# Kernel optimization log

Hardware: AMD Instinct MI355X
Metric: run time of the kernel (lower is better)

Reference implementation:

```python
import jax, jax.numpy as jnp
import numpy as np

B, N_LR, N_HR = 2, 8192, 16384
C = 32          # feature channels (query_ch = neigh_ch = 32 in Grouper7)
NSAMPLE = 64    # nsamples=[64]
RADIUS = 1.0    # radius=[1.0]
LR_VOX = np.array([0.4, 0.4, 1.0], np.float32)   # lr_voxel_size (x,y,z)
HR_VOX = np.array([0.05, 0.05, 0.1], np.float32) # hr_voxel_size (x,y,z)
OFFSET = np.array([0.0, -40.0, -3.0], np.float32)


def setup_inputs() -> dict:
    key = jax.random.key(0)
    ks = jax.random.split(key, 6)
    lr_idx = jax.random.randint(ks[0], (B, N_LR, 3), 0, 25, dtype=jnp.int32)    # (z,y,x) voxel coords
    hr_idx = jax.random.randint(ks[1], (B, N_HR, 3), 0, 200, dtype=jnp.int32)
    lr_feat = jax.random.normal(ks[2], (B, N_LR, C), jnp.float32)
    hr_feat = jax.random.normal(ks[3], (B, N_HR, C), jnp.float32)
    # Grouper7 MLP [[32,32]] on use_xyz-augmented neighbor feats (3+C -> 32 -> 32), bn=False
    W1 = jax.random.normal(ks[4], (C + 3, C), jnp.float32) * 0.1
    b1 = jnp.zeros((C,), jnp.float32)
    W2 = jax.random.normal(ks[5], (C, C), jnp.float32) * 0.1
    b2 = jnp.zeros((C,), jnp.float32)
    return dict(lr_idx=lr_idx, hr_idx=hr_idx, lr_feat=lr_feat, hr_feat=hr_feat,
                W1=W1, b1=b1, W2=W2, b2=b2)


def _to_xyz(idx, vox, off):
    # spconv indices are (z,y,x); code does indices[:, [3,2,1]] * voxel_size + offset + 0.5*voxel_size
    return idx[..., ::-1].astype(jnp.float32) * vox + off + 0.5 * vox


def _group_one(lr_xyz, hr_xyz, hr_f, W1, b1, W2, b2):
    # ball query: first NSAMPLE hr points within RADIUS of each lr query point
    d2 = jnp.sum((lr_xyz[:, None, :] - hr_xyz[None, :, :]) ** 2, axis=-1)  # [N_lr, N_hr]
    mask = d2 <= RADIUS ** 2
    order = jnp.where(mask, -jnp.arange(hr_xyz.shape[0], dtype=jnp.float32), -jnp.inf)
    _, idx = jax.lax.top_k(order, NSAMPLE)            # lowest valid indices first (PointNet++ semantics)
    valid = jnp.take_along_axis(mask, idx, axis=1)
    first = jnp.where(valid[:, :1], idx[:, :1], 0)
    idx = jnp.where(valid, idx, first)                # pad empty slots with first valid neighbor (0 if none)
    rel = hr_xyz[idx] - lr_xyz[:, None, :]            # [N_lr, ns, 3] relative coords (use_xyz=True)
    g = jnp.concatenate([rel, hr_f[idx]], axis=-1)    # [N_lr, ns, 3+C]
    h = jax.nn.relu(g @ W1 + b1)                      # shared 1x1-conv MLP, bn=False
    h = jax.nn.relu(h @ W2 + b2)
    return h.max(axis=1)                              # max-pool over neighbors -> [N_lr, C]


def reference(lr_idx, hr_idx, lr_feat, hr_feat, W1, b1, W2, b2):
    vox_lr = jnp.asarray(LR_VOX)
    vox_hr = jnp.asarray(HR_VOX)
    off = jnp.asarray(OFFSET)
    lr_xyz = _to_xyz(lr_idx, vox_lr, off)             # [B, N_lr, 3]
    hr_xyz = _to_xyz(hr_idx, vox_hr, off)             # [B, N_hr, 3]
    new = jax.vmap(_group_one, in_axes=(0, 0, 0, None, None, None, None))(
        lr_xyz, hr_xyz, hr_feat, W1, b1, W2, b2)      # [B, N_lr, C]
    # structured_forward: torch.cat([lr_features, new_lr_features], dim=-1)
    return jnp.concatenate([lr_feat, new], axis=-1)   # [B, N_lr, 2C]
```

## Files before the change

### kernel.cpp

```cpp
#include <hip/hip_runtime.h>
#include <cstdint>
#include <cstddef>
#include <climits>

constexpr int B_   = 2;
constexpr int NLR  = 8192;
constexpr int NHR  = 16384;
constexpr int CCH  = 32;
constexpr int NS   = 64;
constexpr int THREADS = 256;

constexpr int GX = 11, GY = 11, GZ = 20;
constexpr int NCELLS = GX * GY * GZ;
constexpr int NCT    = B_ * NCELLS;
constexpr int CAP    = 192;
constexpr float SCALE = 0.999f;

__device__ __forceinline__ float cvt_coord(int i, float vox, float off) {
    return __fadd_rn(__fadd_rn(__fmul_rn((float)i, vox), off), __fmul_rn(0.5f, vox));
}

__device__ __forceinline__ void hr_coords(const int* ip, float& x, float& y, float& z) {
    x = cvt_coord(ip[2], 0.05f,   0.0f);
    y = cvt_coord(ip[1], 0.05f, -40.0f);
    z = cvt_coord(ip[0], 0.1f,   -3.0f);
}

__device__ __forceinline__ int cell_of(float x, float y, float z) {
    const int cx = (int)(__fmul_rn(x, SCALE));
    const int cy = (int)(__fmul_rn(__fadd_rn(y, 40.0f), SCALE));
    const int cz = (int)(__fmul_rn(__fadd_rn(z,  3.0f), SCALE));
    return (cz * GY + cy) * GX + cx;
}

extern "C" __global__ void k_hist(const int* __restrict__ hr_idx, int* __restrict__ cnt) {
    const int gid = blockIdx.x * THREADS + threadIdx.x;
    const int b = gid >> 14;
    const int* ip = hr_idx + (size_t)gid * 3;
    float x, y, z;
    hr_coords(ip, x, y, z);
    atomicAdd(&cnt[b * NCELLS + cell_of(x, y, z)], 1);
}

extern "C" __global__ void k_scan(const int* __restrict__ cnt, int* __restrict__ start,
                                  int* __restrict__ cursor) {
    __shared__ int sums[THREADS];
    constexpr int CH = (NCT + THREADS - 1) / THREADS;
    const int t = threadIdx.x;
    int loc[CH];
    int s = 0;
#pragma unroll
    for (int k = 0; k < CH; ++k) {
        const int i = t * CH + k;
        loc[k] = s;
        s += (i < NCT) ? cnt[i] : 0;
    }
    sums[t] = s;
    __syncthreads();
    for (int off = 1; off < THREADS; off <<= 1) {
        const int v = (t >= off) ? sums[t - off] : 0;
        __syncthreads();
        sums[t] += v;
        __syncthreads();
    }
    const int pre = (t > 0) ? sums[t - 1] : 0;
#pragma unroll
    for (int k = 0; k < CH; ++k) {
        const int i = t * CH + k;
        if (i < NCT) {
            const int st = pre + loc[k];
            start[i]  = st;
            cursor[i] = st;
        }
    }
    if (t == THREADS - 1) start[NCT] = sums[THREADS - 1];
}

extern "C" __global__ void k_scatter(const int* __restrict__ hr_idx, int* __restrict__ cursor,
                                     float4* __restrict__ pts) {
    const int gid = blockIdx.x * THREADS + threadIdx.x;
    const int b = gid >> 14;
    const int i = gid & (NHR - 1);
    const int* ip = hr_idx + (size_t)gid * 3;
    float x, y, z;
    hr_coords(ip, x, y, z);
    const int c = b * NCELLS + cell_of(x, y, z);
    const int slot = atomicAdd(&cursor[c], 1);
    float4 v;
    v.x = x; v.y = y; v.z = z; v.w = __int_as_float(i);
    pts[slot] = v;
}

extern "C" __global__ void __launch_bounds__(THREADS)
__attribute__((amdgpu_waves_per_eu(2, 4)))
k_group(const int* __restrict__ lr_idx, const int* __restrict__ hr_idx,
        const float* __restrict__ lr_feat, const float* __restrict__ hr_feat,
        const float* __restrict__ W1, const float* __restrict__ b1,
        const float* __restrict__ W2, const float* __restrict__ b2,
        const int* __restrict__ start, const float4* __restrict__ pts,
        float* __restrict__ out)
{
    __shared__ int cand[4][CAP];

    const int tid  = threadIdx.x;
    const int wave = tid >> 6;
    const int lane = tid & 63;
    const int q    = blockIdx.x * 4 + wave;
    const int b    = q >> 13;

    const int* qip = lr_idx + (size_t)q * 3;
    const float qx = cvt_coord(qip[2], 0.4f,   0.0f);
    const float qy = cvt_coord(qip[1], 0.4f, -40.0f);
    const float qz = cvt_coord(qip[0], 1.0f,  -3.0f);

    const int cqx = (int)(__fmul_rn(qx, SCALE));
    const int cqy = (int)(__fmul_rn(__fadd_rn(qy, 40.0f), SCALE));
    const int cqz = (int)(__fmul_rn(__fadd_rn(qz,  3.0f), SCALE));
    const int x0 = max(cqx - 1, 0), x1 = min(cqx + 1, GX - 1);
    const int y0 = max(cqy - 1, 0), y1 = min(cqy + 1, GY - 1);
    const int z0 = max(cqz - 1, 0), z1 = min(cqz + 1, GZ - 1);
    const int nx = x1 - x0 + 1;
    const int bbase = b * NCELLS;

    int cnt = 0;
    for (int zz = z0; zz <= z1; ++zz)
    for (int yy = y0; yy <= y1; ++yy) {
        const int g0 = bbase + (zz * GY + yy) * GX + x0;
        const int s  = start[g0];
        const int e  = start[g0 + nx];
        for (int base = s; base < e; base += 64) {
            const int j = base + lane;
            bool ok = false;
            int id = 0;
            if (j < e) {
                const float4 pv = pts[j];
                const float dx = __fsub_rn(qx, pv.x);
                const float dy = __fsub_rn(qy, pv.y);
                const float dz = __fsub_rn(qz, pv.z);
                const float d2 = __fadd_rn(__fadd_rn(__fmul_rn(dx, dx),
                                                     __fmul_rn(dy, dy)),
                                           __fmul_rn(dz, dz));
                ok = d2 <= 1.0f;
                id = __float_as_int(pv.w);
            }
            const unsigned long long m = __ballot(ok);
            if (m != 0ull) {
                const int before = (int)__popcll(m & ((1ull << lane) - 1ull));
                const int pos = cnt + before;
                if (ok && pos < CAP) cand[wave][pos] = id;
                cnt += (int)__popcll(m);
                if (cnt > CAP) cnt = CAP;
            }
        }
    }

    int pid;
    if (cnt <= NS) {
        int myid = (lane < cnt) ? cand[wave][lane] : INT_MAX;
        int mp = myid;
#pragma unroll
        for (int s = 32; s >= 1; s >>= 1) mp = min(mp, __shfl_xor(mp, s, 64));
        pid = (lane < cnt) ? myid : ((cnt > 0) ? mp : 0);
    } else {
        const int c = cnt;
        int mine = 0;
        for (int k = 0; k < NS; ++k) {
            int lm = INT_MAX;
            for (int j = lane; j < c; j += 64) lm = min(lm, cand[wave][j]);
#pragma unroll
            for (int s = 32; s >= 1; s >>= 1) lm = min(lm, __shfl_xor(lm, s, 64));
            for (int j = lane; j < c; j += 64)
                if (cand[wave][j] == lm) cand[wave][j] = INT_MAX;
            if (lane == k) mine = lm;
        }
        pid = mine;
    }

    const int* ip = hr_idx + ((size_t)b * NHR + pid) * 3;
    float px, py, pz;
    hr_coords(ip, px, py, pz);

    float g[3 + CCH];
    g[0] = __fsub_rn(px, qx);
    g[1] = __fsub_rn(py, qy);
    g[2] = __fsub_rn(pz, qz);
    const float4* fp = reinterpret_cast<const float4*>(hr_feat + ((size_t)b * NHR + pid) * CCH);
#pragma unroll
    for (int k = 0; k < CCH / 4; ++k) {
        const float4 v = fp[k];
        g[3 + 4 * k + 0] = v.x;
        g[3 + 4 * k + 1] = v.y;
        g[3 + 4 * k + 2] = v.z;
        g[3 + 4 * k + 3] = v.w;
    }

    float h[32];
#pragma unroll 32
    for (int j = 0; j < 32; ++j) h[j] = b1[j];
#pragma unroll 35
    for (int k = 0; k < 35; ++k) {
        const float gk = g[k];
#pragma unroll 32
        for (int j = 0; j < 32; ++j)
            h[j] = fmaf(gk, W1[k * 32 + j], h[j]);
    }
#pragma unroll 32
    for (int j = 0; j < 32; ++j) h[j] = fmaxf(h[j], 0.0f);

    float h2[32];
#pragma unroll 32
    for (int j = 0; j < 32; ++j) h2[j] = b2[j];
#pragma unroll 32
    for (int k = 0; k < 32; ++k) {
        const float hk = h[k];
#pragma unroll 32
        for (int j = 0; j < 32; ++j)
            h2[j] = fmaf(hk, W2[k * 32 + j], h2[j]);
    }
#pragma unroll 32
    for (int j = 0; j < 32; ++j) h2[j] = fmaxf(h2[j], 0.0f);

#pragma unroll
    for (int s = 32; s >= 1; s >>= 1) {
#pragma unroll 32
        for (int j = 0; j < 32; ++j)
            h2[j] = fmaxf(h2[j], __shfl_xor(h2[j], s, 64));
    }

    float* orow = out + (size_t)q * (2 * CCH);
    if (lane < CCH)
        orow[lane] = lr_feat[(size_t)q * CCH + lane];
    if (lane == 0) {
#pragma unroll
        for (int j = 0; j < 8; ++j) {
            float4 v;
            v.x = h2[4 * j + 0];
            v.y = h2[4 * j + 1];
            v.z = h2[4 * j + 2];
            v.w = h2[4 * j + 3];
            reinterpret_cast<float4*>(orow + CCH)[j] = v;
        }
    }
}

extern "C" void kernel_launch(void* const* d_in, const int* in_sizes, int n_in,
                              void* d_out, int out_size, void* d_ws, size_t ws_size,
                              hipStream_t stream) {
    const int*   lr_idx  = (const int*)  d_in[0];
    const int*   hr_idx  = (const int*)  d_in[1];
    const float* lr_feat = (const float*)d_in[2];
    const float* hr_feat = (const float*)d_in[3];
    const float* W1      = (const float*)d_in[4];
    const float* b1      = (const float*)d_in[5];
    const float* W2      = (const float*)d_in[6];
    const float* b2      = (const float*)d_in[7];
    float* out = (float*)d_out;

    int*    cell_count  = (int*)d_ws;
    int*    cell_start  = cell_count + NCT;
    int*    cell_cursor = cell_start + (NCT + 1);
    size_t  off = ((size_t)(3 * NCT + 1) * sizeof(int) + 15) & ~(size_t)15;
    float4* pts = (float4*)((char*)d_ws + off);

    hipMemsetAsync(cell_count, 0, NCT * sizeof(int), stream);

    const dim3 blk(THREADS);
    hipLaunchKernelGGL(k_hist,    dim3(B_ * NHR / THREADS), blk, 0, stream, hr_idx, cell_count);
    hipLaunchKernelGGL(k_scan,    dim3(1),                  blk, 0, stream, cell_count, cell_start, cell_cursor);
    hipLaunchKernelGGL(k_scatter, dim3(B_ * NHR / THREADS), blk, 0, stream, hr_idx, cell_cursor, pts);
    hipLaunchKernelGGL(k_group,   dim3(B_ * NLR / 4),       blk, 0, stream,
                       lr_idx, hr_idx, lr_feat, hr_feat, W1, b1, W2, b2,
                       cell_start, pts, out);
}
```

Before: 177.3 us.

## Run grouper MLP on bf16 MFMA with LDS-staged swizzled operands

Replaces the per-lane scalar FP32 two-layer MLP (35x32 and 32x32 FMAs per neighbor plus a 32-channel shuffle max-reduction) with bf16 16x16x32 MFMA tiles. Weights are converted to bf16 and laid out in LDS in fragment order, and gathered neighbor features and hidden activations are staged in XOR-swizzled LDS buffers. The max-pool then reduces only two values per lane across 4 row groups. This removes most VALU work and register pressure, at the cost of bf16 precision on inputs and activations and more LDS use. The waves-per-eu hint is also dropped.

```diff
diff --git a/kernel.cpp b/kernel.cpp
--- a/kernel.cpp
+++ b/kernel.cpp
@@ -1,4 +1,5 @@
 #include <hip/hip_runtime.h>
+#include <hip/hip_bf16.h>
 #include <cstdint>
 #include <cstddef>
 #include <climits>
@@ -16,6 +17,9 @@
 constexpr int CAP    = 192;
 constexpr float SCALE = 0.999f;
 
+typedef __attribute__((ext_vector_type(8))) short bf16x8;
+typedef __attribute__((ext_vector_type(4))) float f32x4;
+
 __device__ __forceinline__ float cvt_coord(int i, float vox, float off) {
     return __fadd_rn(__fadd_rn(__fmul_rn((float)i, vox), off), __fmul_rn(0.5f, vox));
 }
@@ -31,6 +35,11 @@
     const int cy = (int)(__fmul_rn(__fadd_rn(y, 40.0f), SCALE));
     const int cz = (int)(__fmul_rn(__fadd_rn(z,  3.0f), SCALE));
     return (cz * GY + cy) * GX + cx;
+}
+
+__device__ __forceinline__ unsigned short f2bf(float f) {
+    __hip_bfloat16 h = __float2bfloat16(f);
+    return __builtin_bit_cast(unsigned short, h);
 }
 
 extern "C" __global__ void k_hist(const int* __restrict__ hr_idx, int* __restrict__ cnt) {
@@ -92,7 +101,6 @@
 }
 
 extern "C" __global__ void __launch_bounds__(THREADS)
-__attribute__((amdgpu_waves_per_eu(2, 4)))
 k_group(const int* __restrict__ lr_idx, const int* __restrict__ hr_idx,
         const float* __restrict__ lr_feat, const float* __restrict__ hr_feat,
         const float* __restrict__ W1, const float* __restrict__ b1,
@@ -100,6 +108,11 @@
         const int* __restrict__ start, const float4* __restrict__ pts,
         float* __restrict__ out)
 {
+    __shared__ __align__(16) unsigned short W1f[2][2][64][8];
+    __shared__ __align__(16) unsigned short W2f[2][64][8];
+    __shared__ __align__(16) unsigned short Xf[4][64][32];
+    __shared__ __align__(16) unsigned short XYZ[4][64][4];
+    __shared__ __align__(16) unsigned short Hb[4][64][32];
     __shared__ int cand[4][CAP];
 
     const int tid  = threadIdx.x;
@@ -107,6 +120,32 @@
     const int lane = tid & 63;
     const int q    = blockIdx.x * 4 + wave;
     const int b    = q >> 13;
+
+#pragma unroll
+    for (int e = 0; e < 8; ++e) {
+        const int flat = tid * 8 + e;
+        const int j  = flat & 7;
+        const int l  = (flat >> 3) & 63;
+        const int ct = (flat >> 9) & 1;
+        const int ks = (flat >> 10) & 1;
+        const int kp = ks * 32 + (l >> 4) * 8 + j;
+        const int n  = ct * 16 + (l & 15);
+        float v = 0.0f;
+        if (kp < 32)       v = W1[(kp + 3) * 32 + n];
+        else if (kp < 35)  v = W1[(kp - 32) * 32 + n];
+        W1f[ks][ct][l][j] = f2bf(v);
+    }
+#pragma unroll
+    for (int e = 0; e < 4; ++e) {
+        const int flat = tid * 4 + e;
+        const int j  = flat & 7;
+        const int l  = (flat >> 3) & 63;
+        const int ct = (flat >> 9) & 1;
+        const int k  = (l >> 4) * 8 + j;
+        const int n  = ct * 16 + (l & 15);
+        W2f[ct][l][j] = f2bf(W2[k * 32 + n]);
+    }
+    __syncthreads();
 
     const int* qip = lr_idx + (size_t)q * 3;
     const float qx = cvt_coord(qip[2], 0.4f,   0.0f);
@@ -176,70 +215,123 @@
         pid = mine;
     }
 
-    const int* ip = hr_idx + ((size_t)b * NHR + pid) * 3;
-    float px, py, pz;
-    hr_coords(ip, px, py, pz);
-
-    float g[3 + CCH];
-    g[0] = __fsub_rn(px, qx);
-    g[1] = __fsub_rn(py, qy);
-    g[2] = __fsub_rn(pz, qz);
-    const float4* fp = reinterpret_cast<const float4*>(hr_feat + ((size_t)b * NHR + pid) * CCH);
-#pragma unroll
-    for (int k = 0; k < CCH / 4; ++k) {
-        const float4 v = fp[k];
-        g[3 + 4 * k + 0] = v.x;
-        g[3 + 4 * k + 1] = v.y;
-        g[3 + 4 * k + 2] = v.z;
-        g[3 + 4 * k + 3] = v.w;
-    }
-
-    float h[32];
-#pragma unroll 32
-    for (int j = 0; j < 32; ++j) h[j] = b1[j];
-#pragma unroll 35
-    for (int k = 0; k < 35; ++k) {
-        const float gk = g[k];
-#pragma unroll 32
-        for (int j = 0; j < 32; ++j)
-            h[j] = fmaf(gk, W1[k * 32 + j], h[j]);
-    }
-#pragma unroll 32
-    for (int j = 0; j < 32; ++j) h[j] = fmaxf(h[j], 0.0f);
-
-    float h2[32];
-#pragma unroll 32
-    for (int j = 0; j < 32; ++j) h2[j] = b2[j];
-#pragma unroll 32
-    for (int k = 0; k < 32; ++k) {
-        const float hk = h[k];
-#pragma unroll 32
-        for (int j = 0; j < 32; ++j)
-            h2[j] = fmaf(hk, W2[k * 32 + j], h2[j]);
-    }
-#pragma unroll 32
-    for (int j = 0; j < 32; ++j) h2[j] = fmaxf(h2[j], 0.0f);
-
-#pragma unroll
-    for (int s = 32; s >= 1; s >>= 1) {
-#pragma unroll 32
-        for (int j = 0; j < 32; ++j)
-            h2[j] = fmaxf(h2[j], __shfl_xor(h2[j], s, 64));
-    }
+    {
+        const int* ip = hr_idx + ((size_t)b * NHR + pid) * 3;
+        float px, py, pz;
+        hr_coords(ip, px, py, pz);
+        const int r = lane;
+        ushort4 t;
+        t.x = f2bf(__fsub_rn(px, qx));
+        t.y = f2bf(__fsub_rn(py, qy));
+        t.z = f2bf(__fsub_rn(pz, qz));
+        t.w = 0;
+        *reinterpret_cast<ushort4*>(&XYZ[wave][r][0]) = t;
+        const float4* fp = reinterpret_cast<const float4*>(hr_feat + ((size_t)b * NHR + pid) * CCH);
+#pragma unroll
+        for (int c = 0; c < 4; ++c) {
+            const float4 a = fp[2 * c];
+            const float4 d = fp[2 * c + 1];
+            uint4 u;
+            u.x = (unsigned)f2bf(a.x) | ((unsigned)f2bf(a.y) << 16);
+            u.y = (unsigned)f2bf(a.z) | ((unsigned)f2bf(a.w) << 16);
+            u.z = (unsigned)f2bf(d.x) | ((unsigned)f2bf(d.y) << 16);
+            u.w = (unsigned)f2bf(d.z) | ((unsigned)f2bf(d.w) << 16);
+            const int byteoff = (c * 16) ^ ((r & 3) << 4);
+            *reinterpret_cast<uint4*>(reinterpret_cast<char*>(&Xf[wave][r][0]) + byteoff) = u;
+        }
+    }
+
+    const int hi  = lane >> 4;
+    const int c15 = lane & 15;
+
+    bf16x8 B1[2][2];
+#pragma unroll
+    for (int ks = 0; ks < 2; ++ks)
+#pragma unroll
+        for (int ct = 0; ct < 2; ++ct)
+            B1[ks][ct] = *reinterpret_cast<const bf16x8*>(&W1f[ks][ct][lane][0]);
+
+    const f32x4 zero4 = {0.0f, 0.0f, 0.0f, 0.0f};
+    f32x4 acc[4][2];
+#pragma unroll
+    for (int rt = 0; rt < 4; ++rt) { acc[rt][0] = zero4; acc[rt][1] = zero4; }
+
+#pragma unroll
+    for (int rt = 0; rt < 4; ++rt) {
+        const int row = rt * 16 + c15;
+        const int byteoff = (hi * 16) ^ ((row & 3) << 4);
+        const bf16x8 a0 = *reinterpret_cast<const bf16x8*>(
+            reinterpret_cast<const char*>(&Xf[wave][row][0]) + byteoff);
+        bf16x8 a1 = {0, 0, 0, 0, 0, 0, 0, 0};
+        if (hi == 0) {
+            const ushort4 t = *reinterpret_cast<const ushort4*>(&XYZ[wave][row][0]);
+            a1[0] = (short)t.x; a1[1] = (short)t.y; a1[2] = (short)t.z;
+        }
+#pragma unroll
+        for (int ct = 0; ct < 2; ++ct) {
+            acc[rt][ct] = __builtin_amdgcn_mfma_f32_16x16x32_bf16(a0, B1[0][ct], acc[rt][ct], 0, 0, 0);
+            acc[rt][ct] = __builtin_amdgcn_mfma_f32_16x16x32_bf16(a1, B1[1][ct], acc[rt][ct], 0, 0, 0);
+        }
+    }
+
+    const float bias1_0 = b1[c15];
+    const float bias1_1 = b1[16 + c15];
+#pragma unroll
+    for (int rt = 0; rt < 4; ++rt)
+#pragma unroll
+        for (int ct = 0; ct < 2; ++ct) {
+            const float bb = ct ? bias1_1 : bias1_0;
+#pragma unroll
+            for (int rr = 0; rr < 4; ++rr) {
+                const float v = fmaxf(acc[rt][ct][rr] + bb, 0.0f);
+                const int row = rt * 16 + hi * 4 + rr;
+                const int boff = (ct * 32 + c15 * 2) ^ ((row & 3) << 4);
+                *reinterpret_cast<unsigned short*>(
+                    reinterpret_cast<char*>(&Hb[wave][row][0]) + boff) = f2bf(v);
+            }
+        }
+
+    bf16x8 B2[2];
+#pragma unroll
+    for (int ct = 0; ct < 2; ++ct)
+        B2[ct] = *reinterpret_cast<const bf16x8*>(&W2f[ct][lane][0]);
+
+    f32x4 acc2[4][2];
+#pragma unroll
+    for (int rt = 0; rt < 4; ++rt) { acc2[rt][0] = zero4; acc2[rt][1] = zero4; }
+
+#pragma unroll
+    for (int rt = 0; rt < 4; ++rt) {
+        const int row = rt * 16 + c15;
+        const int byteoff = (hi * 16) ^ ((row & 3) << 4);
+        const bf16x8 a = *reinterpret_cast<const bf16x8*>(
+            reinterpret_cast<const char*>(&Hb[wave][row][0]) + byteoff);
+#pragma unroll
+        for (int ct = 0; ct < 2; ++ct)
+            acc2[rt][ct] = __builtin_amdgcn_mfma_f32_16x16x32_bf16(a, B2[ct], acc2[rt][ct], 0, 0, 0);
+    }
+
+    const float bias2_0 = b2[c15];
+    const float bias2_1 = b2[16 + c15];
+    float m0 = 0.0f, m1 = 0.0f;
+#pragma unroll
+    for (int rt = 0; rt < 4; ++rt)
+#pragma unroll
+        for (int rr = 0; rr < 4; ++rr) {
+            m0 = fmaxf(m0, fmaxf(acc2[rt][0][rr] + bias2_0, 0.0f));
+            m1 = fmaxf(m1, fmaxf(acc2[rt][1][rr] + bias2_1, 0.0f));
+        }
+    m0 = fmaxf(m0, __shfl_xor(m0, 16, 64));
+    m0 = fmaxf(m0, __shfl_xor(m0, 32, 64));
+    m1 = fmaxf(m1, __shfl_xor(m1, 16, 64));
+    m1 = fmaxf(m1, __shfl_xor(m1, 32, 64));
 
     float* orow = out + (size_t)q * (2 * CCH);
     if (lane < CCH)
         orow[lane] = lr_feat[(size_t)q * CCH + lane];
-    if (lane == 0) {
-#pragma unroll
-        for (int j = 0; j < 8; ++j) {
-            float4 v;
-            v.x = h2[4 * j + 0];
-            v.y = h2[4 * j + 1];
-            v.z = h2[4 * j + 2];
-            v.w = h2[4 * j + 3];
-            reinterpret_cast<float4*>(orow + CCH)[j] = v;
-        }
+    if (lane < 16) {
+        orow[CCH + lane]      = m0;
+        orow[CCH + 16 + lane] = m1;
     }
 }
 
```

New measurement: 149.5 us. -15.7%, faster.
